# Kernel tuning notes

Measured on AMD Instinct MI355X. Metric: run time of the kernel, lower is better.

## Reference

```python
import jax, jax.numpy as jnp
import numpy as np
import math

D_MODEL = 512
NHEAD = 8
D_FF = 2048
EPS = 1e-5


def setup_inputs() -> dict:
    key = jax.random.key(0)
    ks = jax.random.split(key, 12)
    B, S, D, F = 8, 1024, D_MODEL, D_FF
    sc_d = 1.0 / math.sqrt(D)
    sc_f = 1.0 / math.sqrt(F)
    return {
        "seq": jax.random.normal(ks[0], (B, S, D), jnp.float32),
        "Wq": jax.random.normal(ks[1], (D, D), jnp.float32) * sc_d,
        "bq": jnp.zeros((D,), jnp.float32),
        "Wk": jax.random.normal(ks[2], (D, D), jnp.float32) * sc_d,
        "bk": jnp.zeros((D,), jnp.float32),
        "Wv": jax.random.normal(ks[3], (D, D), jnp.float32) * sc_d,
        "bv": jnp.zeros((D,), jnp.float32),
        "W1": jax.random.normal(ks[4], (D, F), jnp.float32) * sc_d,
        "b1": jnp.zeros((F,), jnp.float32),
        "W2": jax.random.normal(ks[5], (F, D), jnp.float32) * sc_f,
        "b2": jnp.zeros((D,), jnp.float32),
        "gamma": jnp.ones((D,), jnp.float32),
        "beta": jnp.zeros((D,), jnp.float32),
    }


def _layernorm(x, gamma, beta):
    mu = jnp.mean(x, axis=-1, keepdims=True)
    var = jnp.mean(jnp.square(x - mu), axis=-1, keepdims=True)
    return (x - mu) * jax.lax.rsqrt(var + EPS) * gamma + beta


def reference(seq, Wq, bq, Wk, bk, Wv, bv, W1, b1, W2, b2, gamma, beta):
    B, S, D = seq.shape
    H, Dh = NHEAD, D // NHEAD
    # QKV projections, split into heads: [B, S, H, Dh]
    q = (seq @ Wq + bq).reshape(B, S, H, Dh)
    k = (seq @ Wk + bk).reshape(B, S, H, Dh)
    v = (seq @ Wv + bv).reshape(B, S, H, Dh)
    # scores [B, H, S, S]; NOTE: original applies softmax FIRST, then divides
    # by sqrt(d_model) (quirk of the source module) -- kept faithfully.
    scores = jnp.einsum('bqhd,bkhd->bhqk', q, k)
    attn = jax.nn.softmax(scores, axis=-1) / math.sqrt(D)
    attn_out = jnp.einsum('bhqk,bkhd->bqhd', attn, v).reshape(B, S, D)
    # residual + LayerNorm (dropout is identity at eval)
    out = _layernorm(seq + attn_out, gamma, beta)
    # FFN with LeakyReLU; second residual has NO layernorm in the source.
    ff = jax.nn.leaky_relu(out @ W1 + b1, negative_slope=0.01) @ W2 + b2
    return out + ff
```

## Files before the change

### kernel.cpp

```cpp
#include <hip/hip_runtime.h>

typedef __bf16 bf16;
typedef __bf16 bf16x4 __attribute__((ext_vector_type(4)));
typedef __bf16 bf16x8 __attribute__((ext_vector_type(8)));
typedef float f32x4 __attribute__((ext_vector_type(4)));
typedef float f32x16 __attribute__((ext_vector_type(16)));

#define MFMA16(a, b, c) __builtin_amdgcn_mfma_f32_16x16x32_bf16((a), (b), (c), 0, 0, 0)
#define MFMA32(a, b, c) __builtin_amdgcn_mfma_f32_32x32x16_bf16((a), (b), (c), 0, 0, 0)
#define PLSWAP(a, b) asm("v_permlane32_swap_b32 %0, %1" : "+v"(a), "+v"(b))

typedef const void __attribute__((address_space(1)))* gas1;
typedef void __attribute__((address_space(3)))* las3;
#define ASYNC16(g, l) __builtin_amdgcn_global_load_lds((gas1)(g), (las3)(l), 16, 0, 0)

__device__ __forceinline__ unsigned pk2(float lo, float hi) {
  unsigned short a = __builtin_bit_cast(unsigned short, (bf16)lo);
  unsigned short b = __builtin_bit_cast(unsigned short, (bf16)hi);
  return (unsigned)a | ((unsigned)b << 16);
}

__global__ __launch_bounds__(256) void prep_kernel(
    const float* __restrict__ seq, const float* __restrict__ Wq,
    const float* __restrict__ Wk, const float* __restrict__ Wv,
    const float* __restrict__ W1, const float* __restrict__ W2,
    const float* __restrict__ bq, const float* __restrict__ bk,
    const float* __restrict__ bv, bf16* __restrict__ seq_bf,
    bf16* __restrict__ qkvT, bf16* __restrict__ W1T, bf16* __restrict__ W2T,
    float* __restrict__ bqkv) {
  __shared__ float tile[32][33];
  const int blk = blockIdx.x;
  const int tid = threadIdx.x;

  if (blk < 2048) {
    int i = blk * 256 + tid;
    float4 a = ((const float4*)seq)[2 * i];
    float4 b = ((const float4*)seq)[2 * i + 1];
    bf16x8 v;
    v[0] = (bf16)a.x; v[1] = (bf16)a.y; v[2] = (bf16)a.z; v[3] = (bf16)a.w;
    v[4] = (bf16)b.x; v[5] = (bf16)b.y; v[6] = (bf16)b.z; v[7] = (bf16)b.w;
    ((bf16x8*)seq_bf)[i] = v;
    return;
  }

  const int tx = tid & 31, ty = tid >> 5;
  const float* in;
  bf16* out;
  int N, K, bx, by;
  if (blk < 3840) {
    if (blk < 2816) {
      int t = blk - 2048;
      int which = t >> 8;
      int r = t & 255;
      in = which == 0 ? Wq : (which == 1 ? Wk : Wv);
      out = qkvT + (long)which * 512 * 512;
      N = 512; K = 512;
      bx = r & 15; by = r >> 4;
    } else {
      int t = blk - 2816;
      in = W1; out = W1T; N = 2048; K = 512;
      bx = t & 63; by = t >> 6;
    }
  } else if (blk < 4864) {
    int t = blk - 3840;
    in = W2; out = W2T; N = 512; K = 2048;
    bx = t & 15; by = t >> 4;
  } else {
    int i = (blk - 4864) * 256 + tid;
    if (i < 512) bqkv[i] = bq[i];
    else if (i < 1024) bqkv[i] = bk[i - 512];
    else if (i < 1536) bqkv[i] = bv[i - 1024];
    return;
  }

  int n0 = bx * 32, k0 = by * 32;
#pragma unroll
  for (int i = 0; i < 4; i++) tile[ty + i * 8][tx] = in[(long)(k0 + ty + i * 8) * N + n0 + tx];
  __syncthreads();
#pragma unroll
  for (int i = 0; i < 4; i++)
    out[(long)(n0 + ty + i * 8) * K + k0 + tx] = (bf16)tile[tx][ty + i * 8];
}

template <int ACT, int RESID, int VSPLIT, int BN, int BK, typename OutT>
__global__ __launch_bounds__(256, 2)
void gemm_bt(const bf16* __restrict__ A, const bf16* __restrict__ BT,
             const float* __restrict__ bias, const bf16* __restrict__ resid,
             OutT* __restrict__ C, bf16* __restrict__ vt,
             int K, int lda, int ldb, int ldc, int gx) {
  constexpr int NT = BN / 32;
  constexpr int KF = BK / 32;
  constexpr int CPR = BK / 8;
  constexpr int BK2 = BK * 2;
  __shared__ __align__(16) char As[128 * BK2];
  __shared__ __align__(16) char Bs[BN * BK2];
  const int tid = threadIdx.x;
  const int l = tid & 63, w = tid >> 6;
  const int lrow = l & 15, lhi = l >> 4;
  const int wr = w >> 1, wc = w & 1;
  const int bid = blockIdx.x;
  const int nwg = gridDim.x;
  const int wg = (bid & 7) * (nwg >> 3) + (bid >> 3);
  const long brow = (long)(wg / gx) * 128;
  const long bcol = (long)(wg % gx) * BN;

  f32x4 zero = {0.f, 0.f, 0.f, 0.f};
  f32x4 acc[4][NT];
#pragma unroll
  for (int m = 0; m < 4; m++)
#pragma unroll
    for (int n = 0; n < NT; n++) acc[m][n] = zero;

  for (int kt = 0; kt < K; kt += BK) {
    __syncthreads();
#pragma unroll
    for (int c = 0; c < CPR / 2; c++) {
      int idx = c * 256 + tid;
      int row = idx / CPR;
      int cole = ((idx & (CPR - 1)) ^ (row & (CPR - 1))) * 8;
      ASYNC16(A + (brow + row) * lda + kt + cole, As + idx * 16);
    }
#pragma unroll
    for (int c = 0; c < (BN * CPR) / 256; c++) {
      int idx = c * 256 + tid;
      int row = idx / CPR;
      int cole = ((idx & (CPR - 1)) ^ (row & (CPR - 1))) * 8;
      ASYNC16(BT + (bcol + row) * ldb + kt + cole, Bs + idx * 16);
    }
    __syncthreads();
    bf16x8 af[4][KF], bfr[NT][KF];
#pragma unroll
    for (int m = 0; m < 4; m++) {
      int row = wr * 64 + m * 16 + lrow;
      int base = row * BK2 + lhi * 16;
      int sw = (row & (CPR - 1)) << 4;
#pragma unroll
      for (int kf = 0; kf < KF; kf++)
        af[m][kf] = *(const bf16x8*)(As + ((base + kf * 64) ^ sw));
    }
#pragma unroll
    for (int n = 0; n < NT; n++) {
      int row = wc * (16 * NT) + n * 16 + lrow;
      int base = row * BK2 + lhi * 16;
      int sw = (row & (CPR - 1)) << 4;
#pragma unroll
      for (int kf = 0; kf < KF; kf++)
        bfr[n][kf] = *(const bf16x8*)(Bs + ((base + kf * 64) ^ sw));
    }
#pragma unroll
    for (int m = 0; m < 4; m++)
#pragma unroll
      for (int n = 0; n < NT; n++)
#pragma unroll
        for (int kf = 0; kf < KF; kf++)
          acc[m][n] = MFMA16(af[m][kf], bfr[n][kf], acc[m][n]);
  }

  if (VSPLIT && bcol >= 1024) {
#pragma unroll
    for (int m = 0; m < 4; m++) {
#pragma unroll
      for (int n = 0; n < NT; n++) {
        long col = bcol + wc * (16 * NT) + n * 16 + lrow;
        float bv = bias[col];
        int cc = (int)col - 1024;
        int hh = cc >> 6, dd = cc & 63;
        long row0 = brow + wr * 64 + m * 16 + lhi * 4;
        int b = (int)(row0 >> 10), s0 = (int)(row0 & 1023);
        bf16x4 v4;
#pragma unroll
        for (int r = 0; r < 4; r++) v4[r] = (bf16)(acc[m][n][r] + bv);
        *(bf16x4*)(vt + ((long)(b * 8 + hh) * 64 + dd) * 1024 + s0) = v4;
      }
    }
    return;
  }

#pragma unroll
  for (int m = 0; m < 4; m++) {
#pragma unroll
    for (int n = 0; n < NT; n++) {
      long col = bcol + wc * (16 * NT) + n * 16 + lrow;
      float bv = bias[col];
#pragma unroll
      for (int r = 0; r < 4; r++) {
        long row = brow + wr * 64 + m * 16 + lhi * 4 + r;
        float v = acc[m][n][r] + bv;
        if (ACT) v = v > 0.f ? v : 0.01f * v;
        if (RESID) v += (float)resid[row * ldc + col];
        C[row * ldc + col] = (OutT)v;
      }
    }
  }
}

__global__ __launch_bounds__(256, 2)
void attn_fwd(const bf16* __restrict__ QKV, const bf16* __restrict__ Vtg,
              bf16* __restrict__ attn_out) {
  __shared__ __align__(16) char Ks[2][64 * 128];
  __shared__ __align__(16) char Vs[2][64 * 128];
  const int tid = threadIdx.x;
  const int l = tid & 63, w = tid >> 6;
  const int q = l & 31, hi = l >> 5;
  const int h = blockIdx.x;
  const long rowbase = (long)blockIdx.y * 1024;
  const int q0 = blockIdx.z * 128;
  const float LOG2E = 1.4426950408889634f;

  const bf16* Kb = QKV + 512;
  const bf16* Vb = Vtg + ((long)blockIdx.y * 8 + h) * 64 * 1024;

  auto stage = [&](int buf, int kt) {
#pragma unroll
    for (int c = 0; c < 2; c++) {
      int idx = c * 256 + tid;
      int row = idx >> 3;
      int cole = ((idx & 7) ^ (row & 7)) * 8;
      ASYNC16(Kb + (rowbase + kt * 64 + row) * 1536 + h * 64 + cole, Ks[buf] + idx * 16);
      ASYNC16(Vb + row * 1024 + kt * 64 + cole, Vs[buf] + idx * 16);
    }
  };

  bf16x8 aq[4];
  {
    long qrow = rowbase + q0 + w * 32 + q;
    const bf16* p = QKV + qrow * 1536 + h * 64 + hi * 8;
    aq[0] = *(const bf16x8*)(p);
    aq[1] = *(const bf16x8*)(p + 16);
    aq[2] = *(const bf16x8*)(p + 32);
    aq[3] = *(const bf16x8*)(p + 48);
  }
  asm volatile("" ::"v"(aq[0]), "v"(aq[1]), "v"(aq[2]), "v"(aq[3]));

  f32x16 o0, o1;
#pragma unroll
  for (int i = 0; i < 16; i++) { o0[i] = 0.f; o1[i] = 0.f; }
  float m_run = -1e30f, l_run = 0.f;

  stage(0, 0);
  int cur = 0;

  for (int kt = 0; kt < 16; ++kt) {
    asm volatile("" ::: "memory");
    __builtin_amdgcn_s_barrier();
    asm volatile("" ::: "memory");
    stage(cur ^ 1, (kt + 1) & 15);
    asm volatile("s_waitcnt vmcnt(4)" ::: "memory");
    __builtin_amdgcn_sched_barrier(0);
    __builtin_amdgcn_s_barrier();
    asm volatile("" ::: "memory");

    const char* Kc = Ks[cur];
    const char* Vc = Vs[cur];

    f32x16 s0, s1;
#pragma unroll
    for (int i = 0; i < 16; i++) { s0[i] = 0.f; s1[i] = 0.f; }
    __builtin_amdgcn_s_setprio(1);
#pragma unroll
    for (int t = 0; t < 2; t++) {
      f32x16 c;
#pragma unroll
      for (int i = 0; i < 16; i++) c[i] = 0.f;
      int row = t * 32 + q;
      int sw = (row & 7) << 4;
#pragma unroll
      for (int sd = 0; sd < 4; sd++) {
        bf16x8 kf = *(const bf16x8*)(Kc + ((row * 128 + sd * 32 + hi * 16) ^ sw));
        c = MFMA32(kf, aq[sd], c);
      }
      if (t) s1 = c; else s0 = c;
    }
    __builtin_amdgcn_s_setprio(0);

    float tmax = s0[0];
#pragma unroll
    for (int i = 1; i < 16; i++) tmax = fmaxf(tmax, s0[i]);
#pragma unroll
    for (int i = 0; i < 16; i++) tmax = fmaxf(tmax, s1[i]);
    tmax = fmaxf(tmax, __shfl_xor(tmax, 32));
    float mn = fmaxf(m_run, tmax);
    float al = __builtin_exp2f((m_run - mn) * LOG2E);
    float mh = mn * LOG2E;
    m_run = mn;
    float p0[16], p1[16];
    float ps = 0.f;
#pragma unroll
    for (int i = 0; i < 16; i++) {
      p0[i] = __builtin_exp2f(__builtin_fmaf(s0[i], LOG2E, -mh));
      ps += p0[i];
    }
#pragma unroll
    for (int i = 0; i < 16; i++) {
      p1[i] = __builtin_exp2f(__builtin_fmaf(s1[i], LOG2E, -mh));
      ps += p1[i];
    }
    ps += __shfl_xor(ps, 32);
    l_run = l_run * al + ps;
#pragma unroll
    for (int i = 0; i < 16; i++) { o0[i] *= al; o1[i] *= al; }

    bf16x8 pa[4];
    {
      unsigned a0 = pk2(p0[0], p0[1]), b0 = pk2(p0[4], p0[5]);
      unsigned a1 = pk2(p0[2], p0[3]), b1 = pk2(p0[6], p0[7]);
      unsigned a2 = pk2(p0[8], p0[9]), b2 = pk2(p0[12], p0[13]);
      unsigned a3 = pk2(p0[10], p0[11]), b3 = pk2(p0[14], p0[15]);
      PLSWAP(a0, b0); PLSWAP(a1, b1); PLSWAP(a2, b2); PLSWAP(a3, b3);
      uint4 w0 = {a0, a1, b0, b1};
      uint4 w1 = {a2, a3, b2, b3};
      pa[0] = __builtin_bit_cast(bf16x8, w0);
      pa[1] = __builtin_bit_cast(bf16x8, w1);
      unsigned c0 = pk2(p1[0], p1[1]), d0 = pk2(p1[4], p1[5]);
      unsigned c1 = pk2(p1[2], p1[3]), d1 = pk2(p1[6], p1[7]);
      unsigned c2 = pk2(p1[8], p1[9]), d2 = pk2(p1[12], p1[13]);
      unsigned c3 = pk2(p1[10], p1[11]), d3 = pk2(p1[14], p1[15]);
      PLSWAP(c0, d0); PLSWAP(c1, d1); PLSWAP(c2, d2); PLSWAP(c3, d3);
      uint4 w2 = {c0, c1, d0, d1};
      uint4 w3 = {c2, c3, d2, d3};
      pa[2] = __builtin_bit_cast(bf16x8, w2);
      pa[3] = __builtin_bit_cast(bf16x8, w3);
    }

    __builtin_amdgcn_s_setprio(1);
    {
      int row = q;
      int sw = (row & 7) << 4;
#pragma unroll
      for (int ks = 0; ks < 4; ks++) {
        bf16x8 vf = *(const bf16x8*)(Vc + ((row * 128 + ks * 32 + hi * 16) ^ sw));
        o0 = MFMA32(vf, pa[ks], o0);
      }
      row = 32 + q;
      sw = (row & 7) << 4;
#pragma unroll
      for (int ks = 0; ks < 4; ks++) {
        bf16x8 vf = *(const bf16x8*)(Vc + ((row * 128 + ks * 32 + hi * 16) ^ sw));
        o1 = MFMA32(vf, pa[ks], o1);
      }
    }
    __builtin_amdgcn_s_setprio(0);
    cur ^= 1;
  }

  float fac = 0.044194173824159216f / l_run;
  long qrow = rowbase + q0 + w * 32 + q;
  bf16* op = attn_out + qrow * 512 + h * 64;
#pragma unroll
  for (int t = 0; t < 4; t++) {
    bf16x4 v0, v1;
#pragma unroll
    for (int u = 0; u < 4; u++) {
      v0[u] = (bf16)(o0[4 * t + u] * fac);
      v1[u] = (bf16)(o1[4 * t + u] * fac);
    }
    *(bf16x4*)(op + 8 * t + 4 * hi) = v0;
    *(bf16x4*)(op + 32 + 8 * t + 4 * hi) = v1;
  }
}

__global__ __launch_bounds__(256) void ln_kernel(const float* __restrict__ seq,
                                                 const bf16* __restrict__ attn,
                                                 const float* __restrict__ gamma,
                                                 const float* __restrict__ beta,
                                                 bf16* __restrict__ out) {
  int row = blockIdx.x;
  int tid = threadIdx.x;
  long base = (long)row * 512;
  float x0 = seq[base + tid] + (float)attn[base + tid];
  float x1 = seq[base + 256 + tid] + (float)attn[base + 256 + tid];
  float s = x0 + x1, ss = x0 * x0 + x1 * x1;
#pragma unroll
  for (int mm = 1; mm < 64; mm <<= 1) {
    s += __shfl_xor(s, mm);
    ss += __shfl_xor(ss, mm);
  }
  __shared__ float red[8];
  int w = tid >> 6, l = tid & 63;
  if (l == 0) { red[w] = s; red[4 + w] = ss; }
  __syncthreads();
  s = red[0] + red[1] + red[2] + red[3];
  ss = red[4] + red[5] + red[6] + red[7];
  float mu = s * (1.f / 512.f);
  float var = ss * (1.f / 512.f) - mu * mu;
  float rs = rsqrtf(var + 1e-5f);
  out[base + tid] = (bf16)((x0 - mu) * rs * gamma[tid] + beta[tid]);
  out[base + 256 + tid] = (bf16)((x1 - mu) * rs * gamma[tid + 256] + beta[tid + 256]);
}

extern "C" void kernel_launch(void* const* d_in, const int* in_sizes, int n_in,
                              void* d_out, int out_size, void* d_ws, size_t ws_size,
                              hipStream_t stream) {
  const float* seq = (const float*)d_in[0];
  const float* Wq = (const float*)d_in[1];
  const float* bq = (const float*)d_in[2];
  const float* Wk = (const float*)d_in[3];
  const float* bk = (const float*)d_in[4];
  const float* Wv = (const float*)d_in[5];
  const float* bv = (const float*)d_in[6];
  const float* W1 = (const float*)d_in[7];
  const float* b1 = (const float*)d_in[8];
  const float* W2 = (const float*)d_in[9];
  const float* b2 = (const float*)d_in[10];
  const float* gamma = (const float*)d_in[11];
  const float* beta = (const float*)d_in[12];
  float* out = (float*)d_out;

  char* ws = (char*)d_ws;
  if (ws_size < 89659392u) return;
  bf16* seq_bf = (bf16*)(ws + 0);
  bf16* qkvT = (bf16*)(ws + 8388608);
  bf16* W1T = (bf16*)(ws + 9961472);
  bf16* W2T = (bf16*)(ws + 12058624);
  float* bqkv = (float*)(ws + 14155776);
  bf16* QKV = (bf16*)(ws + 14161920);
  bf16* attn = (bf16*)(ws + 39327744);
  bf16* ln = (bf16*)(ws + 47716352);
  bf16* hidden = (bf16*)(ws + 56104960);
  bf16* vt = (bf16*)(ws + 56104960);

  prep_kernel<<<4870, 256, 0, stream>>>(seq, Wq, Wk, Wv, W1, W2, bq, bk, bv,
                                        seq_bf, qkvT, W1T, W2T, bqkv);

  gemm_bt<0, 0, 1, 128, 64, bf16><<<768, 256, 0, stream>>>(
      seq_bf, qkvT, bqkv, (const bf16*)nullptr, QKV, vt, 512, 512, 512, 1536, 12);
  attn_fwd<<<dim3(8, 8, 8), 256, 0, stream>>>(QKV, vt, attn);
  ln_kernel<<<8192, 256, 0, stream>>>(seq, attn, gamma, beta, ln);
  gemm_bt<1, 0, 0, 128, 64, bf16><<<1024, 256, 0, stream>>>(
      ln, W1T, b1, (const bf16*)nullptr, hidden, (bf16*)nullptr, 512, 512, 512, 2048, 16);
  gemm_bt<0, 1, 0, 64, 128, float><<<512, 256, 0, stream>>>(
      hidden, W2T, b2, ln, out, (bf16*)nullptr, 2048, 2048, 2048, 512, 8);
}
```

Before: 124.8 us.

## Split attention over key halves and merge with a combine kernel

Doubles the attention grid by having each block process only half of the key sequence. Each block writes an unnormalized partial output plus its running max and sum. A new combine kernel rescales the two partials and applies the final normalization. This raises parallelism and occupancy on the GPU, at the cost of an extra kernel launch, extra global traffic for the partials, and reuse of dead workspace buffers.

```diff
diff --git a/kernel.cpp b/kernel.cpp
--- a/kernel.cpp
+++ b/kernel.cpp
@@ -196,7 +196,8 @@
 
 __global__ __launch_bounds__(256, 2)
 void attn_fwd(const bf16* __restrict__ QKV, const bf16* __restrict__ Vtg,
-              bf16* __restrict__ attn_out) {
+              bf16* __restrict__ O1, bf16* __restrict__ O2,
+              float2* __restrict__ ml1, float2* __restrict__ ml2) {
   __shared__ __align__(16) char Ks[2][64 * 128];
   __shared__ __align__(16) char Vs[2][64 * 128];
   const int tid = threadIdx.x;
@@ -204,8 +205,13 @@
   const int q = l & 31, hi = l >> 5;
   const int h = blockIdx.x;
   const long rowbase = (long)blockIdx.y * 1024;
-  const int q0 = blockIdx.z * 128;
+  const int q0 = (blockIdx.z & 7) * 128;
+  const int half = blockIdx.z >> 3;
+  const int kt0 = half * 8;
   const float LOG2E = 1.4426950408889634f;
+
+  bf16* Obuf = half ? O2 : O1;
+  float2* mlp = half ? ml2 : ml1;
 
   const bf16* Kb = QKV + 512;
   const bf16* Vb = Vtg + ((long)blockIdx.y * 8 + h) * 64 * 1024;
@@ -237,14 +243,14 @@
   for (int i = 0; i < 16; i++) { o0[i] = 0.f; o1[i] = 0.f; }
   float m_run = -1e30f, l_run = 0.f;
 
-  stage(0, 0);
+  stage(0, kt0);
   int cur = 0;
 
-  for (int kt = 0; kt < 16; ++kt) {
+  for (int i = 0; i < 8; ++i) {
     asm volatile("" ::: "memory");
     __builtin_amdgcn_s_barrier();
     asm volatile("" ::: "memory");
-    stage(cur ^ 1, (kt + 1) & 15);
+    stage(cur ^ 1, kt0 + ((i + 1) & 7));
     asm volatile("s_waitcnt vmcnt(4)" ::: "memory");
     __builtin_amdgcn_sched_barrier(0);
     __builtin_amdgcn_s_barrier();
@@ -255,13 +261,13 @@
 
     f32x16 s0, s1;
 #pragma unroll
-    for (int i = 0; i < 16; i++) { s0[i] = 0.f; s1[i] = 0.f; }
+    for (int i2 = 0; i2 < 16; i2++) { s0[i2] = 0.f; s1[i2] = 0.f; }
     __builtin_amdgcn_s_setprio(1);
 #pragma unroll
     for (int t = 0; t < 2; t++) {
       f32x16 c;
 #pragma unroll
-      for (int i = 0; i < 16; i++) c[i] = 0.f;
+      for (int i2 = 0; i2 < 16; i2++) c[i2] = 0.f;
       int row = t * 32 + q;
       int sw = (row & 7) << 4;
 #pragma unroll
@@ -275,9 +281,9 @@
 
     float tmax = s0[0];
 #pragma unroll
-    for (int i = 1; i < 16; i++) tmax = fmaxf(tmax, s0[i]);
-#pragma unroll
-    for (int i = 0; i < 16; i++) tmax = fmaxf(tmax, s1[i]);
+    for (int i2 = 1; i2 < 16; i2++) tmax = fmaxf(tmax, s0[i2]);
+#pragma unroll
+    for (int i2 = 0; i2 < 16; i2++) tmax = fmaxf(tmax, s1[i2]);
     tmax = fmaxf(tmax, __shfl_xor(tmax, 32));
     float mn = fmaxf(m_run, tmax);
     float al = __builtin_exp2f((m_run - mn) * LOG2E);
@@ -286,19 +292,19 @@
     float p0[16], p1[16];
     float ps = 0.f;
 #pragma unroll
-    for (int i = 0; i < 16; i++) {
-      p0[i] = __builtin_exp2f(__builtin_fmaf(s0[i], LOG2E, -mh));
-      ps += p0[i];
-    }
-#pragma unroll
-    for (int i = 0; i < 16; i++) {
-      p1[i] = __builtin_exp2f(__builtin_fmaf(s1[i], LOG2E, -mh));
-      ps += p1[i];
+    for (int i2 = 0; i2 < 16; i2++) {
+      p0[i2] = __builtin_exp2f(__builtin_fmaf(s0[i2], LOG2E, -mh));
+      ps += p0[i2];
+    }
+#pragma unroll
+    for (int i2 = 0; i2 < 16; i2++) {
+      p1[i2] = __builtin_exp2f(__builtin_fmaf(s1[i2], LOG2E, -mh));
+      ps += p1[i2];
     }
     ps += __shfl_xor(ps, 32);
     l_run = l_run * al + ps;
 #pragma unroll
-    for (int i = 0; i < 16; i++) { o0[i] *= al; o1[i] *= al; }
+    for (int i2 = 0; i2 < 16; i2++) { o0[i2] *= al; o1[i2] *= al; }
 
     bf16x8 pa[4];
     {
@@ -343,20 +349,49 @@
     cur ^= 1;
   }
 
-  float fac = 0.044194173824159216f / l_run;
   long qrow = rowbase + q0 + w * 32 + q;
-  bf16* op = attn_out + qrow * 512 + h * 64;
+  bf16* op = Obuf + qrow * 512 + h * 64;
 #pragma unroll
   for (int t = 0; t < 4; t++) {
     bf16x4 v0, v1;
 #pragma unroll
     for (int u = 0; u < 4; u++) {
-      v0[u] = (bf16)(o0[4 * t + u] * fac);
-      v1[u] = (bf16)(o1[4 * t + u] * fac);
+      v0[u] = (bf16)o0[4 * t + u];
+      v1[u] = (bf16)o1[4 * t + u];
     }
     *(bf16x4*)(op + 8 * t + 4 * hi) = v0;
     *(bf16x4*)(op + 32 + 8 * t + 4 * hi) = v1;
   }
+  if (hi == 0) {
+    float2 ml;
+    ml.x = m_run;
+    ml.y = l_run;
+    mlp[qrow * 8 + h] = ml;
+  }
+}
+
+__global__ __launch_bounds__(256) void attn_combine(
+    const bf16* __restrict__ O2, const float2* __restrict__ ml1,
+    const float2* __restrict__ ml2, bf16* __restrict__ O1) {
+  const float LOG2E = 1.4426950408889634f;
+  long gid = (long)blockIdx.x * 256 + threadIdx.x;
+  long row = gid >> 6;
+  int cg = (int)(gid & 63);
+  int h = cg >> 3;
+  long base = row * 512 + cg * 8;
+  float2 a = ml1[row * 8 + h];
+  float2 b = ml2[row * 8 + h];
+  float m = fmaxf(a.x, b.x);
+  float w1 = __builtin_exp2f((a.x - m) * LOG2E);
+  float w2 = __builtin_exp2f((b.x - m) * LOG2E);
+  float fac = 0.044194173824159216f / (w1 * a.y + w2 * b.y);
+  bf16x8 v1 = *(const bf16x8*)(O1 + base);
+  bf16x8 v2 = *(const bf16x8*)(O2 + base);
+  bf16x8 o;
+#pragma unroll
+  for (int i = 0; i < 8; i++)
+    o[i] = (bf16)(((float)v1[i] * w1 + (float)v2[i] * w2) * fac);
+  *(bf16x8*)(O1 + base) = o;
 }
 
 __global__ __launch_bounds__(256) void ln_kernel(const float* __restrict__ seq,
@@ -410,6 +445,8 @@
   if (ws_size < 89659392u) return;
   bf16* seq_bf = (bf16*)(ws + 0);
   bf16* qkvT = (bf16*)(ws + 8388608);
+  float2* ml1 = (float2*)(ws + 8388608);
+  float2* ml2 = (float2*)(ws + 8912896);
   bf16* W1T = (bf16*)(ws + 9961472);
   bf16* W2T = (bf16*)(ws + 12058624);
   float* bqkv = (float*)(ws + 14155776);
@@ -424,7 +461,8 @@
 
   gemm_bt<0, 0, 1, 128, 64, bf16><<<768, 256, 0, stream>>>(
       seq_bf, qkvT, bqkv, (const bf16*)nullptr, QKV, vt, 512, 512, 512, 1536, 12);
-  attn_fwd<<<dim3(8, 8, 8), 256, 0, stream>>>(QKV, vt, attn);
+  attn_fwd<<<dim3(8, 8, 16), 256, 0, stream>>>(QKV, vt, attn, seq_bf, ml1, ml2);
+  attn_combine<<<2048, 256, 0, stream>>>(seq_bf, ml1, ml2, attn);
   ln_kernel<<<8192, 256, 0, stream>>>(seq, attn, gamma, beta, ln);
   gemm_bt<1, 0, 0, 128, 64, bf16><<<1024, 256, 0, stream>>>(
       ln, W1T, b1, (const bf16*)nullptr, hidden, (bf16*)nullptr, 512, 512, 512, 2048, 16);
```

New measurement: 130.8 us. 1.05x slower.
